# Kernel optimization log

Hardware: AMD Instinct MI355X
Metric: run time of the kernel (lower is better)

The kernel has to match this reference:

```python
import jax, jax.numpy as jnp
import numpy as np

N_NODES = 50000
N_EDGES = 600000
IN_CH = 64
HID = 128
N_GRAPHS = 64
EPS = 0.0  # GINEConv default eps


def setup_inputs() -> dict:
    key = jax.random.key(0)
    ks = jax.random.split(key, 16)
    x = jax.random.normal(ks[0], (N_NODES, IN_CH), dtype=jnp.float32)
    edge_index = jax.random.randint(ks[1], (2, N_EDGES), 0, N_NODES, dtype=jnp.int64)
    edge_attr = jax.random.normal(ks[2], (N_EDGES, 3), dtype=jnp.float32)
    batch = jnp.sort(jax.random.randint(ks[3], (N_NODES,), 0, N_GRAPHS, dtype=jnp.int64))
    s = lambda fan_in: 1.0 / np.sqrt(fan_in)
    # conv1: edge lin (3->IN_CH), mlp (IN_CH->HID->HID)
    el1_w = jax.random.uniform(ks[4], (3, IN_CH), minval=-s(3), maxval=s(3))
    el1_b = jnp.zeros((IN_CH,), jnp.float32)
    w1a = jax.random.uniform(ks[5], (IN_CH, HID), minval=-s(IN_CH), maxval=s(IN_CH))
    b1a = jnp.zeros((HID,), jnp.float32)
    w1b = jax.random.uniform(ks[6], (HID, HID), minval=-s(HID), maxval=s(HID))
    b1b = jnp.zeros((HID,), jnp.float32)
    # conv2: edge lin (3->HID), mlp (HID->HID->HID)
    el2_w = jax.random.uniform(ks[7], (3, HID), minval=-s(3), maxval=s(3))
    el2_b = jnp.zeros((HID,), jnp.float32)
    w2a = jax.random.uniform(ks[8], (HID, HID), minval=-s(HID), maxval=s(HID))
    b2a = jnp.zeros((HID,), jnp.float32)
    w2b = jax.random.uniform(ks[9], (HID, HID), minval=-s(HID), maxval=s(HID))
    b2b = jnp.zeros((HID,), jnp.float32)
    return dict(x=x, edge_index=edge_index, edge_attr=edge_attr, batch=batch,
                el1_w=el1_w, el1_b=el1_b, w1a=w1a, b1a=b1a, w1b=w1b, b1b=b1b,
                el2_w=el2_w, el2_b=el2_b, w2a=w2a, b2a=b2a, w2b=w2b, b2b=b2b)


def _gine_conv(x, src, dst, edge_attr, el_w, el_b, wa, ba, wb, bb):
    # message: relu(x_j + Lin(edge_attr)), aggregated (sum) at target nodes
    e = edge_attr @ el_w + el_b              # [E, d]
    msg = jax.nn.relu(x[src] + e)            # [E, d]
    agg = jax.ops.segment_sum(msg, dst, num_segments=x.shape[0])  # [N, d]
    h = (1.0 + EPS) * x + agg
    h = jax.nn.relu(h @ wa + ba) @ wb + bb   # MLP
    return h


def reference(x, edge_index, edge_attr, batch,
              el1_w, el1_b, w1a, b1a, w1b, b1b,
              el2_w, el2_b, w2a, b2a, w2b, b2b):
    src, dst = edge_index[0], edge_index[1]
    h = jax.nn.relu(_gine_conv(x, src, dst, edge_attr, el1_w, el1_b, w1a, b1a, w1b, b1b))
    h = jax.nn.relu(_gine_conv(h, src, dst, edge_attr, el2_w, el2_b, w2a, b2a, w2b, b2b))
    # global mean pool per graph
    sums = jax.ops.segment_sum(h, batch, num_segments=N_GRAPHS)
    cnt = jax.ops.segment_sum(jnp.ones((h.shape[0],), h.dtype), batch, num_segments=N_GRAPHS)
    return sums / jnp.maximum(cnt, 1.0)[:, None]
```

## Files before the change

### kernel.cpp

```cpp
#include <hip/hip_runtime.h>

#define N_NODES 50000
#define N_EDGES 600000
#define N_PAD 50048
#define IN_CH 64
#define HID 128
#define N_GRAPHS 64
#define CAP 64
#define CAP_SHIFT 6

typedef __attribute__((ext_vector_type(8))) short bf16x8;
typedef __attribute__((ext_vector_type(4))) float f32x4;

__device__ __forceinline__ float bf2f(unsigned short u) {
    union { unsigned int i; float f; } v; v.i = ((unsigned int)u) << 16; return v.f;
}
__device__ __forceinline__ unsigned short f2bf(float f) {
    union { float f; unsigned int i; } v; v.f = f;
    unsigned int u = v.i;
    return (unsigned short)((u + 0x7FFFu + ((u >> 16) & 1u)) >> 16);
}


__global__ void prep_kernel(const float* __restrict__ x,
                            const float* __restrict__ w1a, const float* __restrict__ w1b,
                            const float* __restrict__ w2a, const float* __restrict__ w2b,
                            unsigned short* __restrict__ xbf,
                            unsigned short* __restrict__ waT1, unsigned short* __restrict__ wbT1,
                            unsigned short* __restrict__ waT2, unsigned short* __restrict__ wbT2,
                            int* __restrict__ deg, float* __restrict__ psum) {
    int i = blockIdx.x * blockDim.x + threadIdx.x;
    if (i < N_NODES * IN_CH) xbf[i] = f2bf(x[i]);
    if (i < N_NODES) deg[i] = 0;
    if (i < N_GRAPHS * HID) psum[i] = 0.f;
    if (i < IN_CH * HID) {
        int k = i / HID, n = i % HID;
        waT1[n * IN_CH + k] = f2bf(w1a[i]);
    }
    if (i < HID * HID) {
        int k = i / HID, n = i % HID;
        wbT1[n * HID + k] = f2bf(w1b[i]);
        waT2[n * HID + k] = f2bf(w2a[i]);
        wbT2[n * HID + k] = f2bf(w2b[i]);
    }
}

__global__ void build_kernel(const int* __restrict__ ei,
                             const float* __restrict__ ea,
                             int* __restrict__ deg,
                             uint2* __restrict__ edata) {
    int i = blockIdx.x * blockDim.x + threadIdx.x;
    if (i >= N_EDGES) return;
    int s = ei[i];
    int d = ei[N_EDGES + i];
    float a0 = ea[3 * (size_t)i], a1 = ea[3 * (size_t)i + 1], a2 = ea[3 * (size_t)i + 2];
    int p = atomicAdd(&deg[d], 1);
    if (p < CAP)
        edata[((size_t)d << CAP_SHIFT) + p] =
            make_uint2((unsigned)s | ((unsigned)f2bf(a0) << 16),
                       (unsigned)f2bf(a1) | ((unsigned)f2bf(a2) << 16));
}

__global__ void gather64_kernel(const unsigned short* __restrict__ xin,
                                const uint2* __restrict__ edata,
                                const int* __restrict__ deg,
                                const float* __restrict__ elw,
                                const float* __restrict__ elb,
                                unsigned short* __restrict__ sg) {
    constexpr int K = IN_CH;
    constexpr int NPB = 4;
    const int node0 = blockIdx.x * NPB;
    const int t = threadIdx.x;
    const int c = t & 63, half = t >> 6;
    const float w0 = elw[c], w1 = elw[K + c], w2 = elw[2 * K + c], eb = elb[c];

    auto term = [&](uint2 e, unsigned short row) -> float {
        float ev = bf2f((unsigned short)(e.x >> 16)) * w0 +
                   bf2f((unsigned short)(e.y & 0xFFFF)) * w1 +
                   bf2f((unsigned short)(e.y >> 16)) * w2 + eb;
        float m = bf2f(row) + ev;
        return m > 0.f ? m : 0.f;
    };

    for (int i = 0; i < NPB; i += 2) {
        int node = node0 + i + half;
        float acc = bf2f(xin[(size_t)node * K + c]);
        int dn = deg[node]; if (dn > CAP) dn = CAP;
        int jb = node << CAP_SHIFT, je = jb + dn;
        int j = jb;
        for (; j + 8 <= je; j += 8) {
            uint2 e0 = edata[j],     e1 = edata[j + 1], e2 = edata[j + 2], e3 = edata[j + 3];
            uint2 e4 = edata[j + 4], e5 = edata[j + 5], e6 = edata[j + 6], e7 = edata[j + 7];
            unsigned short r0 = xin[(size_t)(e0.x & 0xFFFF) * K + c];
            unsigned short r1 = xin[(size_t)(e1.x & 0xFFFF) * K + c];
            unsigned short r2 = xin[(size_t)(e2.x & 0xFFFF) * K + c];
            unsigned short r3 = xin[(size_t)(e3.x & 0xFFFF) * K + c];
            unsigned short r4 = xin[(size_t)(e4.x & 0xFFFF) * K + c];
            unsigned short r5 = xin[(size_t)(e5.x & 0xFFFF) * K + c];
            unsigned short r6 = xin[(size_t)(e6.x & 0xFFFF) * K + c];
            unsigned short r7 = xin[(size_t)(e7.x & 0xFFFF) * K + c];
            acc += term(e0, r0) + term(e1, r1) + term(e2, r2) + term(e3, r3)
                 + term(e4, r4) + term(e5, r5) + term(e6, r6) + term(e7, r7);
        }
        for (; j + 4 <= je; j += 4) {
            uint2 e0 = edata[j], e1 = edata[j + 1], e2 = edata[j + 2], e3 = edata[j + 3];
            unsigned short r0 = xin[(size_t)(e0.x & 0xFFFF) * K + c];
            unsigned short r1 = xin[(size_t)(e1.x & 0xFFFF) * K + c];
            unsigned short r2 = xin[(size_t)(e2.x & 0xFFFF) * K + c];
            unsigned short r3 = xin[(size_t)(e3.x & 0xFFFF) * K + c];
            acc += term(e0, r0) + term(e1, r1) + term(e2, r2) + term(e3, r3);
        }
        for (; j < je; j++) {
            uint2 e0 = edata[j];
            acc += term(e0, xin[(size_t)(e0.x & 0xFFFF) * K + c]);
        }
        sg[(size_t)node * K + c] = f2bf(acc);
    }
}

__global__ void gather128_kernel(const unsigned short* __restrict__ xin,
                                 const uint2* __restrict__ edata,
                                 const int* __restrict__ deg,
                                 const float* __restrict__ elw,
                                 const float* __restrict__ elb,
                                 unsigned short* __restrict__ sg) {
    const int t = threadIdx.x;
    const int w = t >> 6, l = t & 63;
    const unsigned* x32 = (const unsigned*)xin;
    unsigned* sg32 = (unsigned*)sg;
    const int c0 = 2 * l;
    const float w00 = elw[c0],           w01 = elw[c0 + 1];
    const float w10 = elw[HID + c0],     w11 = elw[HID + c0 + 1];
    const float w20 = elw[2 * HID + c0], w21 = elw[2 * HID + c0 + 1];
    const float eb0 = elb[c0],           eb1 = elb[c0 + 1];
    const int nA = (blockIdx.x * 4 + w) * 2;
    const int nB = nA + 1;

    unsigned svA = x32[(size_t)nA * 64 + l];
    unsigned svB = x32[(size_t)nB * 64 + l];
    float a0 = bf2f((unsigned short)(svA & 0xFFFF));
    float a1 = bf2f((unsigned short)(svA >> 16));
    float b0 = bf2f((unsigned short)(svB & 0xFFFF));
    float b1 = bf2f((unsigned short)(svB >> 16));

    auto term2 = [&](uint2 e, unsigned r, float& p0, float& p1) {
        float A0 = bf2f((unsigned short)(e.x >> 16));
        float A1 = bf2f((unsigned short)(e.y & 0xFFFF));
        float A2 = bf2f((unsigned short)(e.y >> 16));
        float ev0 = A0 * w00 + A1 * w10 + A2 * w20 + eb0;
        float ev1 = A0 * w01 + A1 * w11 + A2 * w21 + eb1;
        float m0 = bf2f((unsigned short)(r & 0xFFFF)) + ev0;
        float m1 = bf2f((unsigned short)(r >> 16)) + ev1;
        p0 += m0 > 0.f ? m0 : 0.f;
        p1 += m1 > 0.f ? m1 : 0.f;
    };

    int dA = deg[nA]; if (dA > CAP) dA = CAP;
    int dB = deg[nB]; if (dB > CAP) dB = CAP;
    int ja = nA << CAP_SHIFT; const int jaE = ja + dA;
    int jb = nB << CAP_SHIFT; const int jbE = jb + dB;
    while (ja + 4 <= jaE && jb + 4 <= jbE) {
        uint2 eA0 = edata[ja],     eA1 = edata[ja + 1], eA2 = edata[ja + 2], eA3 = edata[ja + 3];
        uint2 eB0 = edata[jb],     eB1 = edata[jb + 1], eB2 = edata[jb + 2], eB3 = edata[jb + 3];
        unsigned rA0 = x32[(size_t)(eA0.x & 0xFFFF) * 64 + l];
        unsigned rA1 = x32[(size_t)(eA1.x & 0xFFFF) * 64 + l];
        unsigned rA2 = x32[(size_t)(eA2.x & 0xFFFF) * 64 + l];
        unsigned rA3 = x32[(size_t)(eA3.x & 0xFFFF) * 64 + l];
        unsigned rB0 = x32[(size_t)(eB0.x & 0xFFFF) * 64 + l];
        unsigned rB1 = x32[(size_t)(eB1.x & 0xFFFF) * 64 + l];
        unsigned rB2 = x32[(size_t)(eB2.x & 0xFFFF) * 64 + l];
        unsigned rB3 = x32[(size_t)(eB3.x & 0xFFFF) * 64 + l];
        term2(eA0, rA0, a0, a1); term2(eA1, rA1, a0, a1);
        term2(eA2, rA2, a0, a1); term2(eA3, rA3, a0, a1);
        term2(eB0, rB0, b0, b1); term2(eB1, rB1, b0, b1);
        term2(eB2, rB2, b0, b1); term2(eB3, rB3, b0, b1);
        ja += 4; jb += 4;
    }
    for (; ja + 4 <= jaE; ja += 4) {
        uint2 e0 = edata[ja], e1 = edata[ja + 1], e2 = edata[ja + 2], e3 = edata[ja + 3];
        unsigned r0 = x32[(size_t)(e0.x & 0xFFFF) * 64 + l];
        unsigned r1 = x32[(size_t)(e1.x & 0xFFFF) * 64 + l];
        unsigned r2 = x32[(size_t)(e2.x & 0xFFFF) * 64 + l];
        unsigned r3 = x32[(size_t)(e3.x & 0xFFFF) * 64 + l];
        term2(e0, r0, a0, a1); term2(e1, r1, a0, a1);
        term2(e2, r2, a0, a1); term2(e3, r3, a0, a1);
    }
    for (; ja < jaE; ja++) {
        uint2 e0 = edata[ja];
        term2(e0, x32[(size_t)(e0.x & 0xFFFF) * 64 + l], a0, a1);
    }
    for (; jb + 4 <= jbE; jb += 4) {
        uint2 e0 = edata[jb], e1 = edata[jb + 1], e2 = edata[jb + 2], e3 = edata[jb + 3];
        unsigned r0 = x32[(size_t)(e0.x & 0xFFFF) * 64 + l];
        unsigned r1 = x32[(size_t)(e1.x & 0xFFFF) * 64 + l];
        unsigned r2 = x32[(size_t)(e2.x & 0xFFFF) * 64 + l];
        unsigned r3 = x32[(size_t)(e3.x & 0xFFFF) * 64 + l];
        term2(e0, r0, b0, b1); term2(e1, r1, b0, b1);
        term2(e2, r2, b0, b1); term2(e3, r3, b0, b1);
    }
    for (; jb < jbE; jb++) {
        uint2 e0 = edata[jb];
        term2(e0, x32[(size_t)(e0.x & 0xFFFF) * 64 + l], b0, b1);
    }
    sg32[(size_t)nA * 64 + l] = (unsigned)f2bf(a0) | ((unsigned)f2bf(a1) << 16);
    sg32[(size_t)nB * 64 + l] = (unsigned)f2bf(b0) | ((unsigned)f2bf(b1) << 16);
}

template <int K, bool POOL>
__global__ __launch_bounds__(256)
void mlp_mfma_kernel(const unsigned short* __restrict__ sg,
                     const unsigned short* __restrict__ waT,
                     const float* __restrict__ ba,
                     const unsigned short* __restrict__ wbT,
                     const float* __restrict__ bb,
                     void* __restrict__ outv,
                     const int* __restrict__ batch) {
    constexpr int HSTR = 136;
    constexpr int OSTR = HID + 4;
    __shared__ __align__(16) unsigned short sHid[4][16 * HSTR];
    __shared__ __align__(16) float sOut[64 * OSTR];
    const int t = threadIdx.x;
    const int w = t >> 6, l = t & 63;
    const int i16 = l & 15, q = l >> 4;
    const int blk0 = blockIdx.x * 64;
    const int row0 = blk0 + w * 16;

    bf16x8 aA[K / 32];
    #pragma unroll
    for (int s = 0; s < K / 32; s++)
        aA[s] = *(const bf16x8*)&sg[(size_t)(row0 + i16) * K + s * 32 + q * 8];
    unsigned short* myHid = sHid[w];
    #pragma unroll
    for (int ct = 0; ct < 8; ct++) {
        int col = ct * 16 + i16;
        float bv = ba[col];
        f32x4 acc = (f32x4){bv, bv, bv, bv};
        #pragma unroll
        for (int s = 0; s < K / 32; s++) {
            bf16x8 b = *(const bf16x8*)&waT[(size_t)col * K + s * 32 + q * 8];
            acc = __builtin_amdgcn_mfma_f32_16x16x32_bf16(aA[s], b, acc, 0, 0, 0);
        }
        #pragma unroll
        for (int r = 0; r < 4; r++) {
            float v = acc[r] > 0.f ? acc[r] : 0.f;
            myHid[(q * 4 + r) * HSTR + col] = f2bf(v);
        }
    }
    __syncthreads();

    bf16x8 aB[4];
    #pragma unroll
    for (int s = 0; s < 4; s++)
        aB[s] = *(const bf16x8*)&myHid[i16 * HSTR + s * 32 + q * 8];
    #pragma unroll
    for (int ct = 0; ct < 8; ct++) {
        int col = ct * 16 + i16;
        float bv = bb[col];
        f32x4 acc = (f32x4){bv, bv, bv, bv};
        #pragma unroll
        for (int s = 0; s < 4; s++) {
            bf16x8 b = *(const bf16x8*)&wbT[(size_t)col * HID + s * 32 + q * 8];
            acc = __builtin_amdgcn_mfma_f32_16x16x32_bf16(aB[s], b, acc, 0, 0, 0);
        }
        #pragma unroll
        for (int r = 0; r < 4; r++) {
            float v = acc[r] > 0.f ? acc[r] : 0.f;
            sOut[(w * 16 + q * 4 + r) * OSTR + col] = v;
        }
    }
    __syncthreads();

    if (POOL) {
        if (t < HID) {
            float* psum = (float*)outv;
            float acc = 0.f;
            int curg = batch[blk0];
            for (int row = 0; row < 64; row++) {
                int node = blk0 + row;
                if (node >= N_NODES) break;
                int g = batch[node];
                if (g != curg) {
                    atomicAdd(&psum[curg * HID + t], acc);
                    acc = 0.f; curg = g;
                }
                acc += sOut[row * OSTR + t];
            }
            atomicAdd(&psum[curg * HID + t], acc);
        }
    } else {
        unsigned short* hout = (unsigned short*)outv;
        for (int idx = t; idx < 64 * 16; idx += 256) {
            int row = idx >> 4, ch = idx & 15;
            int node = blk0 + row;
            if (node < N_NODES) {
                float4 f0 = *(const float4*)&sOut[row * OSTR + ch * 8];
                float4 f1 = *(const float4*)&sOut[row * OSTR + ch * 8 + 4];
                uint4 u;
                u.x = (unsigned)f2bf(f0.x) | ((unsigned)f2bf(f0.y) << 16);
                u.y = (unsigned)f2bf(f0.z) | ((unsigned)f2bf(f0.w) << 16);
                u.z = (unsigned)f2bf(f1.x) | ((unsigned)f2bf(f1.y) << 16);
                u.w = (unsigned)f2bf(f1.z) | ((unsigned)f2bf(f1.w) << 16);
                *(uint4*)&hout[(size_t)node * HID + ch * 8] = u;
            }
        }
    }
}

__global__ void pool_div_kernel(const float* __restrict__ sums,
                                const int* __restrict__ batch,
                                float* __restrict__ out) {
    int i = blockIdx.x * blockDim.x + threadIdx.x;
    if (i >= N_GRAPHS * HID) return;
    int g = i / HID;
    int lo = 0, hi = N_NODES;
    while (lo < hi) { int mid = (lo + hi) >> 1; if (batch[mid] < g) lo = mid + 1; else hi = mid; }
    int start = lo;
    lo = 0; hi = N_NODES;
    while (lo < hi) { int mid = (lo + hi) >> 1; if (batch[mid] <= g) lo = mid + 1; else hi = mid; }
    float c = (float)(lo - start);
    out[i] = sums[i] / (c > 1.0f ? c : 1.0f);
}

extern "C" void kernel_launch(void* const* d_in, const int* in_sizes, int n_in,
                              void* d_out, int out_size, void* d_ws, size_t ws_size,
                              hipStream_t stream) {
    const float* x    = (const float*)d_in[0];
    const int*   ei   = (const int*)d_in[1];
    const float* ea   = (const float*)d_in[2];
    const int*   batch= (const int*)d_in[3];
    const float* el1w = (const float*)d_in[4];
    const float* el1b = (const float*)d_in[5];
    const float* w1a  = (const float*)d_in[6];
    const float* b1a  = (const float*)d_in[7];
    const float* w1b  = (const float*)d_in[8];
    const float* b1b  = (const float*)d_in[9];
    const float* el2w = (const float*)d_in[10];
    const float* el2b = (const float*)d_in[11];
    const float* w2a  = (const float*)d_in[12];
    const float* b2a  = (const float*)d_in[13];
    const float* w2b  = (const float*)d_in[14];
    const float* b2b  = (const float*)d_in[15];
    float* out = (float*)d_out;

    uint2* edata    = (uint2*)d_ws;
    float* psum     = (float*)(edata + (size_t)N_NODES * CAP);
    int*   deg      = (int*)(psum + N_GRAPHS * HID);
    unsigned short* hbf  = (unsigned short*)((char*)psum + (size_t)58192 * 4);
    unsigned short* sgbuf= hbf + (size_t)N_NODES * HID;
    unsigned short* waT1 = sgbuf + (size_t)N_PAD * HID;
    unsigned short* wbT1 = waT1 + HID * IN_CH;
    unsigned short* waT2 = wbT1 + HID * HID;
    unsigned short* wbT2 = waT2 + HID * HID;
    unsigned short* xbf  = wbT2 + HID * HID;

    prep_kernel<<<(N_NODES * IN_CH) / 256, 256, 0, stream>>>(
        x, w1a, w1b, w2a, w2b, xbf, waT1, wbT1, waT2, wbT2, deg, psum);
    build_kernel<<<(N_EDGES + 255) / 256, 256, 0, stream>>>(ei, ea, deg, edata);

    gather64_kernel<<<N_NODES / 4, 128, 0, stream>>>(
        xbf, edata, deg, el1w, el1b, sgbuf);
    mlp_mfma_kernel<IN_CH, false><<<N_PAD / 64, 256, 0, stream>>>(
        sgbuf, waT1, b1a, wbT1, b1b, hbf, nullptr);

    gather128_kernel<<<N_NODES / 8, 256, 0, stream>>>(
        hbf, edata, deg, el2w, el2b, sgbuf);
    mlp_mfma_kernel<HID, true><<<N_PAD / 64, 256, 0, stream>>>(
        sgbuf, waT2, b2a, wbT2, b2b, psum, batch);

    pool_div_kernel<<<(N_GRAPHS * HID + 255) / 256, 256, 0, stream>>>(psum, batch, out);
}
```

Before: 268.7 us.

## Fuse all stages into one persistent cooperative kernel with grid syncs

Replaces seven separate kernel launches (prep, CSR build, two gathers, two MLPs, pool divide) with a single cooperative persistent kernel that runs each stage as a grid-stride loop separated by grid.sync(). The goal is to remove per-launch overhead and inter-kernel gaps. In exchange, the grid is limited to resident blocks (occupancy times 256 CUs). Grid-wide barriers and lower parallelism in the gather phases may slow those phases, and the shared LDS buffer now needs extra block barriers in the MLP tile.

```diff
diff --git a/kernel.cpp b/kernel.cpp
--- a/kernel.cpp
+++ b/kernel.cpp
@@ -1,4 +1,7 @@
 #include <hip/hip_runtime.h>
+#include <hip/hip_cooperative_groups.h>
+
+namespace cg = cooperative_groups;
 
 #define N_NODES 50000
 #define N_EDGES 600000
@@ -8,6 +11,7 @@
 #define N_GRAPHS 64
 #define CAP 64
 #define CAP_SHIFT 6
+#define N_TILES (N_PAD / 64)
 
 typedef __attribute__((ext_vector_type(8))) short bf16x8;
 typedef __attribute__((ext_vector_type(4))) float f32x4;
@@ -22,214 +26,31 @@
 }
 
 
-__global__ void prep_kernel(const float* __restrict__ x,
-                            const float* __restrict__ w1a, const float* __restrict__ w1b,
-                            const float* __restrict__ w2a, const float* __restrict__ w2b,
-                            unsigned short* __restrict__ xbf,
-                            unsigned short* __restrict__ waT1, unsigned short* __restrict__ wbT1,
-                            unsigned short* __restrict__ waT2, unsigned short* __restrict__ wbT2,
-                            int* __restrict__ deg, float* __restrict__ psum) {
-    int i = blockIdx.x * blockDim.x + threadIdx.x;
-    if (i < N_NODES * IN_CH) xbf[i] = f2bf(x[i]);
-    if (i < N_NODES) deg[i] = 0;
-    if (i < N_GRAPHS * HID) psum[i] = 0.f;
-    if (i < IN_CH * HID) {
-        int k = i / HID, n = i % HID;
-        waT1[n * IN_CH + k] = f2bf(w1a[i]);
-    }
-    if (i < HID * HID) {
-        int k = i / HID, n = i % HID;
-        wbT1[n * HID + k] = f2bf(w1b[i]);
-        waT2[n * HID + k] = f2bf(w2a[i]);
-        wbT2[n * HID + k] = f2bf(w2b[i]);
-    }
-}
-
-__global__ void build_kernel(const int* __restrict__ ei,
-                             const float* __restrict__ ea,
-                             int* __restrict__ deg,
-                             uint2* __restrict__ edata) {
-    int i = blockIdx.x * blockDim.x + threadIdx.x;
-    if (i >= N_EDGES) return;
-    int s = ei[i];
-    int d = ei[N_EDGES + i];
-    float a0 = ea[3 * (size_t)i], a1 = ea[3 * (size_t)i + 1], a2 = ea[3 * (size_t)i + 2];
-    int p = atomicAdd(&deg[d], 1);
-    if (p < CAP)
-        edata[((size_t)d << CAP_SHIFT) + p] =
-            make_uint2((unsigned)s | ((unsigned)f2bf(a0) << 16),
-                       (unsigned)f2bf(a1) | ((unsigned)f2bf(a2) << 16));
-}
-
-__global__ void gather64_kernel(const unsigned short* __restrict__ xin,
-                                const uint2* __restrict__ edata,
-                                const int* __restrict__ deg,
-                                const float* __restrict__ elw,
-                                const float* __restrict__ elb,
-                                unsigned short* __restrict__ sg) {
-    constexpr int K = IN_CH;
-    constexpr int NPB = 4;
-    const int node0 = blockIdx.x * NPB;
-    const int t = threadIdx.x;
-    const int c = t & 63, half = t >> 6;
-    const float w0 = elw[c], w1 = elw[K + c], w2 = elw[2 * K + c], eb = elb[c];
-
-    auto term = [&](uint2 e, unsigned short row) -> float {
-        float ev = bf2f((unsigned short)(e.x >> 16)) * w0 +
-                   bf2f((unsigned short)(e.y & 0xFFFF)) * w1 +
-                   bf2f((unsigned short)(e.y >> 16)) * w2 + eb;
-        float m = bf2f(row) + ev;
-        return m > 0.f ? m : 0.f;
-    };
-
-    for (int i = 0; i < NPB; i += 2) {
-        int node = node0 + i + half;
-        float acc = bf2f(xin[(size_t)node * K + c]);
-        int dn = deg[node]; if (dn > CAP) dn = CAP;
-        int jb = node << CAP_SHIFT, je = jb + dn;
-        int j = jb;
-        for (; j + 8 <= je; j += 8) {
-            uint2 e0 = edata[j],     e1 = edata[j + 1], e2 = edata[j + 2], e3 = edata[j + 3];
-            uint2 e4 = edata[j + 4], e5 = edata[j + 5], e6 = edata[j + 6], e7 = edata[j + 7];
-            unsigned short r0 = xin[(size_t)(e0.x & 0xFFFF) * K + c];
-            unsigned short r1 = xin[(size_t)(e1.x & 0xFFFF) * K + c];
-            unsigned short r2 = xin[(size_t)(e2.x & 0xFFFF) * K + c];
-            unsigned short r3 = xin[(size_t)(e3.x & 0xFFFF) * K + c];
-            unsigned short r4 = xin[(size_t)(e4.x & 0xFFFF) * K + c];
-            unsigned short r5 = xin[(size_t)(e5.x & 0xFFFF) * K + c];
-            unsigned short r6 = xin[(size_t)(e6.x & 0xFFFF) * K + c];
-            unsigned short r7 = xin[(size_t)(e7.x & 0xFFFF) * K + c];
-            acc += term(e0, r0) + term(e1, r1) + term(e2, r2) + term(e3, r3)
-                 + term(e4, r4) + term(e5, r5) + term(e6, r6) + term(e7, r7);
-        }
-        for (; j + 4 <= je; j += 4) {
-            uint2 e0 = edata[j], e1 = edata[j + 1], e2 = edata[j + 2], e3 = edata[j + 3];
-            unsigned short r0 = xin[(size_t)(e0.x & 0xFFFF) * K + c];
-            unsigned short r1 = xin[(size_t)(e1.x & 0xFFFF) * K + c];
-            unsigned short r2 = xin[(size_t)(e2.x & 0xFFFF) * K + c];
-            unsigned short r3 = xin[(size_t)(e3.x & 0xFFFF) * K + c];
-            acc += term(e0, r0) + term(e1, r1) + term(e2, r2) + term(e3, r3);
-        }
-        for (; j < je; j++) {
-            uint2 e0 = edata[j];
-            acc += term(e0, xin[(size_t)(e0.x & 0xFFFF) * K + c]);
-        }
-        sg[(size_t)node * K + c] = f2bf(acc);
-    }
-}
-
-__global__ void gather128_kernel(const unsigned short* __restrict__ xin,
-                                 const uint2* __restrict__ edata,
-                                 const int* __restrict__ deg,
-                                 const float* __restrict__ elw,
-                                 const float* __restrict__ elb,
-                                 unsigned short* __restrict__ sg) {
-    const int t = threadIdx.x;
-    const int w = t >> 6, l = t & 63;
-    const unsigned* x32 = (const unsigned*)xin;
-    unsigned* sg32 = (unsigned*)sg;
-    const int c0 = 2 * l;
-    const float w00 = elw[c0],           w01 = elw[c0 + 1];
-    const float w10 = elw[HID + c0],     w11 = elw[HID + c0 + 1];
-    const float w20 = elw[2 * HID + c0], w21 = elw[2 * HID + c0 + 1];
-    const float eb0 = elb[c0],           eb1 = elb[c0 + 1];
-    const int nA = (blockIdx.x * 4 + w) * 2;
-    const int nB = nA + 1;
-
-    unsigned svA = x32[(size_t)nA * 64 + l];
-    unsigned svB = x32[(size_t)nB * 64 + l];
-    float a0 = bf2f((unsigned short)(svA & 0xFFFF));
-    float a1 = bf2f((unsigned short)(svA >> 16));
-    float b0 = bf2f((unsigned short)(svB & 0xFFFF));
-    float b1 = bf2f((unsigned short)(svB >> 16));
-
-    auto term2 = [&](uint2 e, unsigned r, float& p0, float& p1) {
-        float A0 = bf2f((unsigned short)(e.x >> 16));
-        float A1 = bf2f((unsigned short)(e.y & 0xFFFF));
-        float A2 = bf2f((unsigned short)(e.y >> 16));
-        float ev0 = A0 * w00 + A1 * w10 + A2 * w20 + eb0;
-        float ev1 = A0 * w01 + A1 * w11 + A2 * w21 + eb1;
-        float m0 = bf2f((unsigned short)(r & 0xFFFF)) + ev0;
-        float m1 = bf2f((unsigned short)(r >> 16)) + ev1;
-        p0 += m0 > 0.f ? m0 : 0.f;
-        p1 += m1 > 0.f ? m1 : 0.f;
-    };
-
-    int dA = deg[nA]; if (dA > CAP) dA = CAP;
-    int dB = deg[nB]; if (dB > CAP) dB = CAP;
-    int ja = nA << CAP_SHIFT; const int jaE = ja + dA;
-    int jb = nB << CAP_SHIFT; const int jbE = jb + dB;
-    while (ja + 4 <= jaE && jb + 4 <= jbE) {
-        uint2 eA0 = edata[ja],     eA1 = edata[ja + 1], eA2 = edata[ja + 2], eA3 = edata[ja + 3];
-        uint2 eB0 = edata[jb],     eB1 = edata[jb + 1], eB2 = edata[jb + 2], eB3 = edata[jb + 3];
-        unsigned rA0 = x32[(size_t)(eA0.x & 0xFFFF) * 64 + l];
-        unsigned rA1 = x32[(size_t)(eA1.x & 0xFFFF) * 64 + l];
-        unsigned rA2 = x32[(size_t)(eA2.x & 0xFFFF) * 64 + l];
-        unsigned rA3 = x32[(size_t)(eA3.x & 0xFFFF) * 64 + l];
-        unsigned rB0 = x32[(size_t)(eB0.x & 0xFFFF) * 64 + l];
-        unsigned rB1 = x32[(size_t)(eB1.x & 0xFFFF) * 64 + l];
-        unsigned rB2 = x32[(size_t)(eB2.x & 0xFFFF) * 64 + l];
-        unsigned rB3 = x32[(size_t)(eB3.x & 0xFFFF) * 64 + l];
-        term2(eA0, rA0, a0, a1); term2(eA1, rA1, a0, a1);
-        term2(eA2, rA2, a0, a1); term2(eA3, rA3, a0, a1);
-        term2(eB0, rB0, b0, b1); term2(eB1, rB1, b0, b1);
-        term2(eB2, rB2, b0, b1); term2(eB3, rB3, b0, b1);
-        ja += 4; jb += 4;
-    }
-    for (; ja + 4 <= jaE; ja += 4) {
-        uint2 e0 = edata[ja], e1 = edata[ja + 1], e2 = edata[ja + 2], e3 = edata[ja + 3];
-        unsigned r0 = x32[(size_t)(e0.x & 0xFFFF) * 64 + l];
-        unsigned r1 = x32[(size_t)(e1.x & 0xFFFF) * 64 + l];
-        unsigned r2 = x32[(size_t)(e2.x & 0xFFFF) * 64 + l];
-        unsigned r3 = x32[(size_t)(e3.x & 0xFFFF) * 64 + l];
-        term2(e0, r0, a0, a1); term2(e1, r1, a0, a1);
-        term2(e2, r2, a0, a1); term2(e3, r3, a0, a1);
-    }
-    for (; ja < jaE; ja++) {
-        uint2 e0 = edata[ja];
-        term2(e0, x32[(size_t)(e0.x & 0xFFFF) * 64 + l], a0, a1);
-    }
-    for (; jb + 4 <= jbE; jb += 4) {
-        uint2 e0 = edata[jb], e1 = edata[jb + 1], e2 = edata[jb + 2], e3 = edata[jb + 3];
-        unsigned r0 = x32[(size_t)(e0.x & 0xFFFF) * 64 + l];
-        unsigned r1 = x32[(size_t)(e1.x & 0xFFFF) * 64 + l];
-        unsigned r2 = x32[(size_t)(e2.x & 0xFFFF) * 64 + l];
-        unsigned r3 = x32[(size_t)(e3.x & 0xFFFF) * 64 + l];
-        term2(e0, r0, b0, b1); term2(e1, r1, b0, b1);
-        term2(e2, r2, b0, b1); term2(e3, r3, b0, b1);
-    }
-    for (; jb < jbE; jb++) {
-        uint2 e0 = edata[jb];
-        term2(e0, x32[(size_t)(e0.x & 0xFFFF) * 64 + l], b0, b1);
-    }
-    sg32[(size_t)nA * 64 + l] = (unsigned)f2bf(a0) | ((unsigned)f2bf(a1) << 16);
-    sg32[(size_t)nB * 64 + l] = (unsigned)f2bf(b0) | ((unsigned)f2bf(b1) << 16);
-}
+#define HSTR 136
+#define OSTR (HID + 4)
+#define LDS_BYTES (64 * OSTR * 4)
 
 template <int K, bool POOL>
-__global__ __launch_bounds__(256)
-void mlp_mfma_kernel(const unsigned short* __restrict__ sg,
-                     const unsigned short* __restrict__ waT,
-                     const float* __restrict__ ba,
-                     const unsigned short* __restrict__ wbT,
-                     const float* __restrict__ bb,
-                     void* __restrict__ outv,
-                     const int* __restrict__ batch) {
-    constexpr int HSTR = 136;
-    constexpr int OSTR = HID + 4;
-    __shared__ __align__(16) unsigned short sHid[4][16 * HSTR];
-    __shared__ __align__(16) float sOut[64 * OSTR];
+__device__ __forceinline__ void mlp_tile(char* lds, int blk0,
+                                         const unsigned short* __restrict__ sg,
+                                         const unsigned short* __restrict__ waT,
+                                         const float* __restrict__ ba,
+                                         const unsigned short* __restrict__ wbT,
+                                         const float* __restrict__ bb,
+                                         void* __restrict__ outv,
+                                         const int* __restrict__ batch) {
+    unsigned short* sHid = (unsigned short*)lds;
+    float* sOut = (float*)lds;
     const int t = threadIdx.x;
     const int w = t >> 6, l = t & 63;
     const int i16 = l & 15, q = l >> 4;
-    const int blk0 = blockIdx.x * 64;
     const int row0 = blk0 + w * 16;
 
     bf16x8 aA[K / 32];
     #pragma unroll
     for (int s = 0; s < K / 32; s++)
         aA[s] = *(const bf16x8*)&sg[(size_t)(row0 + i16) * K + s * 32 + q * 8];
-    unsigned short* myHid = sHid[w];
+    unsigned short* myHid = sHid + w * (16 * HSTR);
     #pragma unroll
     for (int ct = 0; ct < 8; ct++) {
         int col = ct * 16 + i16;
@@ -246,12 +67,12 @@
             myHid[(q * 4 + r) * HSTR + col] = f2bf(v);
         }
     }
-    __syncthreads();
 
     bf16x8 aB[4];
     #pragma unroll
     for (int s = 0; s < 4; s++)
         aB[s] = *(const bf16x8*)&myHid[i16 * HSTR + s * 32 + q * 8];
+    __syncthreads();
     #pragma unroll
     for (int ct = 0; ct < 8; ct++) {
         int col = ct * 16 + i16;
@@ -304,21 +125,212 @@
             }
         }
     }
-}
-
-__global__ void pool_div_kernel(const float* __restrict__ sums,
-                                const int* __restrict__ batch,
-                                float* __restrict__ out) {
-    int i = blockIdx.x * blockDim.x + threadIdx.x;
-    if (i >= N_GRAPHS * HID) return;
-    int g = i / HID;
-    int lo = 0, hi = N_NODES;
-    while (lo < hi) { int mid = (lo + hi) >> 1; if (batch[mid] < g) lo = mid + 1; else hi = mid; }
-    int start = lo;
-    lo = 0; hi = N_NODES;
-    while (lo < hi) { int mid = (lo + hi) >> 1; if (batch[mid] <= g) lo = mid + 1; else hi = mid; }
-    float c = (float)(lo - start);
-    out[i] = sums[i] / (c > 1.0f ? c : 1.0f);
+    __syncthreads();
+}
+
+__global__ __launch_bounds__(256, 4)
+void gine_coop_kernel(const float* __restrict__ x,
+                      const int* __restrict__ ei,
+                      const float* __restrict__ ea,
+                      const int* __restrict__ batch,
+                      const float* __restrict__ el1w, const float* __restrict__ el1b,
+                      const float* __restrict__ b1a,  const float* __restrict__ b1b,
+                      const float* __restrict__ el2w, const float* __restrict__ el2b,
+                      const float* __restrict__ b2a,  const float* __restrict__ b2b,
+                      const float* __restrict__ w1a,  const float* __restrict__ w1b,
+                      const float* __restrict__ w2a,  const float* __restrict__ w2b,
+                      uint2* __restrict__ edata, int* __restrict__ deg,
+                      float* __restrict__ psum,
+                      unsigned short* __restrict__ xbf,
+                      unsigned short* __restrict__ sgbuf,
+                      unsigned short* __restrict__ hbf,
+                      unsigned short* __restrict__ waT1, unsigned short* __restrict__ wbT1,
+                      unsigned short* __restrict__ waT2, unsigned short* __restrict__ wbT2,
+                      float* __restrict__ out) {
+    __shared__ __align__(16) char lds[LDS_BYTES];
+    cg::grid_group grid = cg::this_grid();
+
+    const int t = threadIdx.x;
+    const int gtid = blockIdx.x * blockDim.x + t;
+    const int GSZ = gridDim.x * blockDim.x;
+    const int w = t >> 6, l = t & 63;
+    const int unit = blockIdx.x * 4 + w;
+    const int NUNITS = gridDim.x * 4;
+
+    for (int i = gtid; i < N_NODES * IN_CH; i += GSZ) {
+        xbf[i] = f2bf(x[i]);
+        if (i < N_NODES) deg[i] = 0;
+        if (i < N_GRAPHS * HID) psum[i] = 0.f;
+        if (i < IN_CH * HID) {
+            int k = i / HID, n = i % HID;
+            waT1[n * IN_CH + k] = f2bf(w1a[i]);
+        }
+        if (i < HID * HID) {
+            int k = i / HID, n = i % HID;
+            wbT1[n * HID + k] = f2bf(w1b[i]);
+            waT2[n * HID + k] = f2bf(w2a[i]);
+            wbT2[n * HID + k] = f2bf(w2b[i]);
+        }
+    }
+    grid.sync();
+
+    for (int i = gtid; i < N_EDGES; i += GSZ) {
+        int s = ei[i];
+        int d = ei[N_EDGES + i];
+        float a0 = ea[3 * (size_t)i], a1 = ea[3 * (size_t)i + 1], a2 = ea[3 * (size_t)i + 2];
+        int p = atomicAdd(&deg[d], 1);
+        if (p < CAP)
+            edata[((size_t)d << CAP_SHIFT) + p] =
+                make_uint2((unsigned)s | ((unsigned)f2bf(a0) << 16),
+                           (unsigned)f2bf(a1) | ((unsigned)f2bf(a2) << 16));
+    }
+    grid.sync();
+
+    {
+        constexpr int K = IN_CH;
+        const int c = l;
+        const float w0 = el1w[c], w1 = el1w[K + c], w2 = el1w[2 * K + c], eb = el1b[c];
+        auto term = [&](uint2 e, unsigned short row) -> float {
+            float ev = bf2f((unsigned short)(e.x >> 16)) * w0 +
+                       bf2f((unsigned short)(e.y & 0xFFFF)) * w1 +
+                       bf2f((unsigned short)(e.y >> 16)) * w2 + eb;
+            float m = bf2f(row) + ev;
+            return m > 0.f ? m : 0.f;
+        };
+        for (int node = unit; node < N_NODES; node += NUNITS) {
+            float acc = bf2f(xbf[(size_t)node * K + c]);
+            int dn = deg[node]; if (dn > CAP) dn = CAP;
+            int j = node << CAP_SHIFT; const int je = j + dn;
+            for (; j + 8 <= je; j += 8) {
+                uint2 e0 = edata[j],     e1 = edata[j + 1], e2 = edata[j + 2], e3 = edata[j + 3];
+                uint2 e4 = edata[j + 4], e5 = edata[j + 5], e6 = edata[j + 6], e7 = edata[j + 7];
+                unsigned short r0 = xbf[(size_t)(e0.x & 0xFFFF) * K + c];
+                unsigned short r1 = xbf[(size_t)(e1.x & 0xFFFF) * K + c];
+                unsigned short r2 = xbf[(size_t)(e2.x & 0xFFFF) * K + c];
+                unsigned short r3 = xbf[(size_t)(e3.x & 0xFFFF) * K + c];
+                unsigned short r4 = xbf[(size_t)(e4.x & 0xFFFF) * K + c];
+                unsigned short r5 = xbf[(size_t)(e5.x & 0xFFFF) * K + c];
+                unsigned short r6 = xbf[(size_t)(e6.x & 0xFFFF) * K + c];
+                unsigned short r7 = xbf[(size_t)(e7.x & 0xFFFF) * K + c];
+                acc += term(e0, r0) + term(e1, r1) + term(e2, r2) + term(e3, r3)
+                     + term(e4, r4) + term(e5, r5) + term(e6, r6) + term(e7, r7);
+            }
+            for (; j + 4 <= je; j += 4) {
+                uint2 e0 = edata[j], e1 = edata[j + 1], e2 = edata[j + 2], e3 = edata[j + 3];
+                unsigned short r0 = xbf[(size_t)(e0.x & 0xFFFF) * K + c];
+                unsigned short r1 = xbf[(size_t)(e1.x & 0xFFFF) * K + c];
+                unsigned short r2 = xbf[(size_t)(e2.x & 0xFFFF) * K + c];
+                unsigned short r3 = xbf[(size_t)(e3.x & 0xFFFF) * K + c];
+                acc += term(e0, r0) + term(e1, r1) + term(e2, r2) + term(e3, r3);
+            }
+            for (; j < je; j++) {
+                uint2 e0 = edata[j];
+                acc += term(e0, xbf[(size_t)(e0.x & 0xFFFF) * K + c]);
+            }
+            sgbuf[(size_t)node * K + c] = f2bf(acc);
+        }
+    }
+    grid.sync();
+
+    for (int tile = blockIdx.x; tile < N_TILES; tile += gridDim.x)
+        mlp_tile<IN_CH, false>(lds, tile * 64, sgbuf, waT1, b1a, wbT1, b1b, hbf, batch);
+    grid.sync();
+
+    {
+        const unsigned* x32 = (const unsigned*)hbf;
+        unsigned* sg32 = (unsigned*)sgbuf;
+        const int c0 = 2 * l;
+        const float w00 = el2w[c0],           w01 = el2w[c0 + 1];
+        const float w10 = el2w[HID + c0],     w11 = el2w[HID + c0 + 1];
+        const float w20 = el2w[2 * HID + c0], w21 = el2w[2 * HID + c0 + 1];
+        const float eb0 = el2b[c0],           eb1 = el2b[c0 + 1];
+        auto term2 = [&](uint2 e, unsigned r, float& p0, float& p1) {
+            float A0 = bf2f((unsigned short)(e.x >> 16));
+            float A1 = bf2f((unsigned short)(e.y & 0xFFFF));
+            float A2 = bf2f((unsigned short)(e.y >> 16));
+            float ev0 = A0 * w00 + A1 * w10 + A2 * w20 + eb0;
+            float ev1 = A0 * w01 + A1 * w11 + A2 * w21 + eb1;
+            float m0 = bf2f((unsigned short)(r & 0xFFFF)) + ev0;
+            float m1 = bf2f((unsigned short)(r >> 16)) + ev1;
+            p0 += m0 > 0.f ? m0 : 0.f;
+            p1 += m1 > 0.f ? m1 : 0.f;
+        };
+        for (int p = unit; p < N_NODES / 2; p += NUNITS) {
+            int nA = 2 * p, nB = 2 * p + 1;
+            unsigned svA = x32[(size_t)nA * 64 + l];
+            unsigned svB = x32[(size_t)nB * 64 + l];
+            float a0 = bf2f((unsigned short)(svA & 0xFFFF));
+            float a1 = bf2f((unsigned short)(svA >> 16));
+            float b0 = bf2f((unsigned short)(svB & 0xFFFF));
+            float b1 = bf2f((unsigned short)(svB >> 16));
+
+            int dA = deg[nA]; if (dA > CAP) dA = CAP;
+            int dB = deg[nB]; if (dB > CAP) dB = CAP;
+            int ja = nA << CAP_SHIFT; const int jaE = ja + dA;
+            int jb = nB << CAP_SHIFT; const int jbE = jb + dB;
+            while (ja + 4 <= jaE && jb + 4 <= jbE) {
+                uint2 eA0 = edata[ja],     eA1 = edata[ja + 1], eA2 = edata[ja + 2], eA3 = edata[ja + 3];
+                uint2 eB0 = edata[jb],     eB1 = edata[jb + 1], eB2 = edata[jb + 2], eB3 = edata[jb + 3];
+                unsigned rA0 = x32[(size_t)(eA0.x & 0xFFFF) * 64 + l];
+                unsigned rA1 = x32[(size_t)(eA1.x & 0xFFFF) * 64 + l];
+                unsigned rA2 = x32[(size_t)(eA2.x & 0xFFFF) * 64 + l];
+                unsigned rA3 = x32[(size_t)(eA3.x & 0xFFFF) * 64 + l];
+                unsigned rB0 = x32[(size_t)(eB0.x & 0xFFFF) * 64 + l];
+                unsigned rB1 = x32[(size_t)(eB1.x & 0xFFFF) * 64 + l];
+                unsigned rB2 = x32[(size_t)(eB2.x & 0xFFFF) * 64 + l];
+                unsigned rB3 = x32[(size_t)(eB3.x & 0xFFFF) * 64 + l];
+                term2(eA0, rA0, a0, a1); term2(eA1, rA1, a0, a1);
+                term2(eA2, rA2, a0, a1); term2(eA3, rA3, a0, a1);
+                term2(eB0, rB0, b0, b1); term2(eB1, rB1, b0, b1);
+                term2(eB2, rB2, b0, b1); term2(eB3, rB3, b0, b1);
+                ja += 4; jb += 4;
+            }
+            for (; ja + 4 <= jaE; ja += 4) {
+                uint2 e0 = edata[ja], e1 = edata[ja + 1], e2 = edata[ja + 2], e3 = edata[ja + 3];
+                unsigned r0 = x32[(size_t)(e0.x & 0xFFFF) * 64 + l];
+                unsigned r1 = x32[(size_t)(e1.x & 0xFFFF) * 64 + l];
+                unsigned r2 = x32[(size_t)(e2.x & 0xFFFF) * 64 + l];
+                unsigned r3 = x32[(size_t)(e3.x & 0xFFFF) * 64 + l];
+                term2(e0, r0, a0, a1); term2(e1, r1, a0, a1);
+                term2(e2, r2, a0, a1); term2(e3, r3, a0, a1);
+            }
+            for (; ja < jaE; ja++) {
+                uint2 e0 = edata[ja];
+                term2(e0, x32[(size_t)(e0.x & 0xFFFF) * 64 + l], a0, a1);
+            }
+            for (; jb + 4 <= jbE; jb += 4) {
+                uint2 e0 = edata[jb], e1 = edata[jb + 1], e2 = edata[jb + 2], e3 = edata[jb + 3];
+                unsigned r0 = x32[(size_t)(e0.x & 0xFFFF) * 64 + l];
+                unsigned r1 = x32[(size_t)(e1.x & 0xFFFF) * 64 + l];
+                unsigned r2 = x32[(size_t)(e2.x & 0xFFFF) * 64 + l];
+                unsigned r3 = x32[(size_t)(e3.x & 0xFFFF) * 64 + l];
+                term2(e0, r0, b0, b1); term2(e1, r1, b0, b1);
+                term2(e2, r2, b0, b1); term2(e3, r3, b0, b1);
+            }
+            for (; jb < jbE; jb++) {
+                uint2 e0 = edata[jb];
+                term2(e0, x32[(size_t)(e0.x & 0xFFFF) * 64 + l], b0, b1);
+            }
+            sg32[(size_t)nA * 64 + l] = (unsigned)f2bf(a0) | ((unsigned)f2bf(a1) << 16);
+            sg32[(size_t)nB * 64 + l] = (unsigned)f2bf(b0) | ((unsigned)f2bf(b1) << 16);
+        }
+    }
+    grid.sync();
+
+    for (int tile = blockIdx.x; tile < N_TILES; tile += gridDim.x)
+        mlp_tile<HID, true>(lds, tile * 64, sgbuf, waT2, b2a, wbT2, b2b, psum, batch);
+    grid.sync();
+
+    for (int i = gtid; i < N_GRAPHS * HID; i += GSZ) {
+        int g = i / HID;
+        int lo = 0, hi = N_NODES;
+        while (lo < hi) { int mid = (lo + hi) >> 1; if (batch[mid] < g) lo = mid + 1; else hi = mid; }
+        int start = lo;
+        lo = 0; hi = N_NODES;
+        while (lo < hi) { int mid = (lo + hi) >> 1; if (batch[mid] <= g) lo = mid + 1; else hi = mid; }
+        float c = (float)(lo - start);
+        out[i] = psum[i] / (c > 1.0f ? c : 1.0f);
+    }
 }
 
 extern "C" void kernel_launch(void* const* d_in, const int* in_sizes, int n_in,
@@ -353,19 +365,26 @@
     unsigned short* wbT2 = waT2 + HID * HID;
     unsigned short* xbf  = wbT2 + HID * HID;
 
-    prep_kernel<<<(N_NODES * IN_CH) / 256, 256, 0, stream>>>(
-        x, w1a, w1b, w2a, w2b, xbf, waT1, wbT1, waT2, wbT2, deg, psum);
-    build_kernel<<<(N_EDGES + 255) / 256, 256, 0, stream>>>(ei, ea, deg, edata);
-
-    gather64_kernel<<<N_NODES / 4, 128, 0, stream>>>(
-        xbf, edata, deg, el1w, el1b, sgbuf);
-    mlp_mfma_kernel<IN_CH, false><<<N_PAD / 64, 256, 0, stream>>>(
-        sgbuf, waT1, b1a, wbT1, b1b, hbf, nullptr);
-
-    gather128_kernel<<<N_NODES / 8, 256, 0, stream>>>(
-        hbf, edata, deg, el2w, el2b, sgbuf);
-    mlp_mfma_kernel<HID, true><<<N_PAD / 64, 256, 0, stream>>>(
-        sgbuf, waT2, b2a, wbT2, b2b, psum, batch);
-
-    pool_div_kernel<<<(N_GRAPHS * HID + 255) / 256, 256, 0, stream>>>(psum, batch, out);
-}
+    static int nblk = 0;
+    if (nblk == 0) {
+        int bpc = 0;
+        hipError_t e = hipOccupancyMaxActiveBlocksPerMultiprocessor(
+            &bpc, gine_coop_kernel, 256, 0);
+        if (e != hipSuccess || bpc < 1) bpc = 1;
+        if (bpc > 8) bpc = 8;
+        nblk = bpc * 256;
+    }
+
+    void* args[] = {
+        (void*)&x, (void*)&ei, (void*)&ea, (void*)&batch,
+        (void*)&el1w, (void*)&el1b, (void*)&b1a, (void*)&b1b,
+        (void*)&el2w, (void*)&el2b, (void*)&b2a, (void*)&b2b,
+        (void*)&w1a, (void*)&w1b, (void*)&w2a, (void*)&w2b,
+        (void*)&edata, (void*)&deg, (void*)&psum,
+        (void*)&xbf, (void*)&sgbuf, (void*)&hbf,
+        (void*)&waT1, (void*)&wbT1, (void*)&waT2, (void*)&wbT2,
+        (void*)&out
+    };
+    hipLaunchCooperativeKernel((void*)gine_coop_kernel, dim3(nblk), dim3(256),
+                               args, 0, stream);
+}
```

Result: slower. 685.4 us (+155.1%).
